# Kernel optimization log

Hardware: AMD Instinct MI355X
Metric: run time of the kernel (lower is better)

The kernel has to match this reference:

```python
import jax, jax.numpy as jnp
import numpy as np

NUM_EXPERTS = 256
TOP_K = 8
N_GROUP = 8
TOPK_GROUP = 4
ROUTED_SCALING = 2.5
EXPERTS_PER_GROUP = NUM_EXPERTS // N_GROUP  # 32


def setup_inputs() -> dict:
    key = jax.random.key(0)
    k1, k2, k3 = jax.random.split(key, 3)
    hidden_states = jax.random.normal(k1, (8192, 7168), dtype=jnp.float32)
    weight = jax.random.normal(k2, (NUM_EXPERTS, 7168), dtype=jnp.float32) * 0.02
    e_score_correction_bias = jax.random.normal(k3, (NUM_EXPERTS,), dtype=jnp.float32) * 0.1
    return {
        "hidden_states": hidden_states,
        "weight": weight,
        "e_score_correction_bias": e_score_correction_bias,
    }


def reference(hidden_states, weight, e_score_correction_bias):
    # Router logits: [T, E]
    router_logits = jnp.einsum("th,eh->te", hidden_states, weight)
    scores = jax.nn.sigmoid(router_logits)
    scores_for_choice = scores + e_score_correction_bias  # [T, E]

    T = scores_for_choice.shape[0]
    # Group-limited selection (noaux_tc): group score = sum of top-2 experts in group
    grouped = scores_for_choice.reshape(T, N_GROUP, EXPERTS_PER_GROUP)
    group_top2, _ = jax.lax.top_k(grouped, 2)            # [T, G, 2]
    group_scores = group_top2.sum(axis=-1)               # [T, G]
    _, group_idx = jax.lax.top_k(group_scores, TOPK_GROUP)  # [T, topk_group]
    group_mask = jax.nn.one_hot(group_idx, N_GROUP, dtype=scores.dtype).max(axis=1)  # [T, G]
    expert_mask = jnp.repeat(group_mask, EXPERTS_PER_GROUP, axis=-1)  # [T, E]
    masked_scores = scores_for_choice * expert_mask

    # Final top-k experts; routing weights gathered from raw sigmoid scores
    _, selected_experts = jax.lax.top_k(masked_scores, TOP_K)         # [T, K] int32
    routing_weights = jnp.take_along_axis(scores, selected_experts, axis=-1)  # [T, K]
    routing_weights = routing_weights / (routing_weights.sum(axis=-1, keepdims=True) + 1e-20)
    routing_weights = routing_weights * ROUTED_SCALING
    return routing_weights, selected_experts
```

## Files before the change

kernel.cpp:

```cpp
#include <hip/hip_runtime.h>
#include <math.h>
#include <stdint.h>

#define T_TOK 8192
#define NEXP  256
#define HD    7168
#define PLANE ((size_t)T_TOK * NEXP)
#define SCALE 4096.0f
#define INV_S2 (1.0f / 16777216.0f)
#define BM 128
#define BK 32
#define NSTEP_TOT (HD / BK)
#define BIMG_STEP 32768

typedef _Float16 h8  __attribute__((ext_vector_type(8)));
typedef float f32x16 __attribute__((ext_vector_type(16)));
typedef __attribute__((address_space(3))) uint8_t       lds_t;
typedef __attribute__((address_space(1))) const uint8_t gbl_t;

__global__ __launch_bounds__(256) void wconv(const float* __restrict__ W,
                                             _Float16* __restrict__ img) {
  const int cc  = blockIdx.x * 256 + threadIdx.x;
  const int t   = cc >> 11;
  const int c   = cc & 2047;
  const int hl  = c >> 10;
  const int rem = c & 1023;
  const int row = rem >> 2;
  const int sp  = rem & 3;
  const int sl  = sp ^ ((row >> 1) & 3);
  const int k   = t * BK + sl * 8;

  const float* src = W + (size_t)row * HD + k;
  const float4 v0 = *(const float4*)src;
  const float4 v1 = *(const float4*)(src + 4);
  const float xs[8] = {v0.x, v0.y, v0.z, v0.w, v1.x, v1.y, v1.z, v1.w};
  h8 out;
#pragma unroll
  for (int j = 0; j < 8; ++j) {
    const float v = xs[j] * SCALE;
    const _Float16 hh = (_Float16)v;
    out[j] = hl ? (_Float16)(v - (float)hh) : hh;
  }
  *(h8*)(img + (size_t)cc * 8) = out;
}

__global__ __launch_bounds__(512, 2) void router_gemm(
    const float* __restrict__ X, const _Float16* __restrict__ img,
    float* __restrict__ partial, int S) {
  __shared__ __align__(1024) _Float16 As[2][2][BM][BK];
  __shared__ __align__(1024) _Float16 Bs[2][2][NEXP][BK];

  const int tid = threadIdx.x;
  const int id  = blockIdx.x;
  const int sb  = id % S;
  const int mb  = id / S;

  const int row0  = mb * BM;
  const int nstep = (HD / S) / BK;
  const int tbase = sb * nstep;

  const int lane = tid & 63, wv = tid >> 6;
  const int wm = wv >> 2, wn = wv & 3;
  const int r31 = lane & 31, kg = lane >> 5;

  const int sm = tid >> 2;
  const int sk = tid & 3;
  const int spA = sk ^ ((sm >> 1) & 3);

  const float* Ap = X + (size_t)(row0 + sm) * HD + tbase * BK + sk * 8;
  const uint8_t* imgB = (const uint8_t*)img + (size_t)tbase * BIMG_STEP + tid * 16;

  f32x16 accP[2][2], accQ[2][2];
#pragma unroll
  for (int i = 0; i < 2; ++i)
#pragma unroll
    for (int j = 0; j < 2; ++j) { accP[i][j] = (f32x16)(0.f); accQ[i][j] = (f32x16)(0.f); }

#define STAGE_B(t, b)                                                          \
  {                                                                            \
    const uint8_t* g = imgB + (size_t)(t) * BIMG_STEP;                         \
    uint8_t* l = (uint8_t*)&Bs[b][0][0][0] + tid * 16;                         \
    _Pragma("unroll")                                                          \
    for (int i = 0; i < 4; ++i)                                                \
      __builtin_amdgcn_global_load_lds((gbl_t*)(uintptr_t)(g + i * 8192),      \
                                       (lds_t*)(uintptr_t)(l + i * 8192),      \
                                       16, 0, 0);                              \
  }

#define CVT_WRITE_A(b, va, vb)                                                 \
  {                                                                            \
    const float xs[8] = {va.x, va.y, va.z, va.w, vb.x, vb.y, vb.z, vb.w};      \
    h8 hv, lv_;                                                                \
    _Pragma("unroll")                                                          \
    for (int j = 0; j < 8; ++j) {                                              \
      const float v = xs[j] * SCALE;                                           \
      const _Float16 hh = (_Float16)v;                                         \
      hv[j] = hh; lv_[j] = (_Float16)(v - (float)hh);                          \
    }                                                                          \
    *(h8*)&As[b][0][sm][spA * 8] = hv;                                         \
    *(h8*)&As[b][1][sm][spA * 8] = lv_;                                        \
  }

  {
    const float4 a0 = *(const float4*)(Ap);
    const float4 a1 = *(const float4*)(Ap + 4);
    __builtin_amdgcn_sched_barrier(0);
    STAGE_B(0, 0);
    asm volatile("s_waitcnt vmcnt(0)" ::: "memory");
    __builtin_amdgcn_sched_barrier(0);
    CVT_WRITE_A(0, a0, a1);
    asm volatile("s_waitcnt lgkmcnt(0)" ::: "memory");
    __builtin_amdgcn_s_barrier();
  }

  for (int t = 0; t < nstep; ++t) {
    const int cur = t & 1;
    const int nxt = cur ^ 1;
    const bool more = (t + 1 < nstep);

    float4 a0, a1;
    if (more) {
      const float* ap = Ap + (size_t)(t + 1) * BK;
      a0 = *(const float4*)(ap);
      a1 = *(const float4*)(ap + 4);
      __builtin_amdgcn_sched_barrier(0);
      STAGE_B(t + 1, nxt);
      __builtin_amdgcn_sched_barrier(0);
      asm volatile("s_waitcnt vmcnt(6)" ::: "memory");
    } else {
      asm volatile("s_waitcnt vmcnt(0)" ::: "memory");
    }
    __builtin_amdgcn_sched_barrier(0);

    h8 aH[2][2], aL[2][2], bH[2][2], bL[2][2];
#pragma unroll
    for (int ks = 0; ks < 2; ++ks) {
#pragma unroll
      for (int mi = 0; mi < 2; ++mi) {
        const int row = wm * 64 + mi * 32 + r31;
        const int sp  = (ks * 2 + kg) ^ ((row >> 1) & 3);
        aH[ks][mi] = *(const h8*)&As[cur][0][row][sp * 8];
        aL[ks][mi] = *(const h8*)&As[cur][1][row][sp * 8];
      }
#pragma unroll
      for (int ni = 0; ni < 2; ++ni) {
        const int col = wn * 64 + ni * 32 + r31;
        const int sp  = (ks * 2 + kg) ^ ((col >> 1) & 3);
        bH[ks][ni] = *(const h8*)&Bs[cur][0][col][sp * 8];
        bL[ks][ni] = *(const h8*)&Bs[cur][1][col][sp * 8];
      }
    }
    asm volatile("s_waitcnt lgkmcnt(0)" ::: "memory");
    __builtin_amdgcn_sched_barrier(0);

    __builtin_amdgcn_s_setprio(1);
#pragma unroll
    for (int ks = 0; ks < 2; ++ks) {
#pragma unroll
      for (int mi = 0; mi < 2; ++mi)
#pragma unroll
        for (int ni = 0; ni < 2; ++ni)
          accP[mi][ni] = __builtin_amdgcn_mfma_f32_32x32x16_f16(aH[ks][mi], bH[ks][ni], accP[mi][ni], 0, 0, 0);
#pragma unroll
      for (int mi = 0; mi < 2; ++mi)
#pragma unroll
        for (int ni = 0; ni < 2; ++ni)
          accQ[mi][ni] = __builtin_amdgcn_mfma_f32_32x32x16_f16(aL[ks][mi], bH[ks][ni], accQ[mi][ni], 0, 0, 0);
#pragma unroll
      for (int mi = 0; mi < 2; ++mi)
#pragma unroll
        for (int ni = 0; ni < 2; ++ni)
          accQ[mi][ni] = __builtin_amdgcn_mfma_f32_32x32x16_f16(aH[ks][mi], bL[ks][ni], accQ[mi][ni], 0, 0, 0);
    }
    __builtin_amdgcn_s_setprio(0);

    if (more) {
      asm volatile("s_waitcnt vmcnt(4)" ::: "memory");
      __builtin_amdgcn_sched_barrier(0);
      CVT_WRITE_A(nxt, a0, a1);
    }
    asm volatile("s_waitcnt lgkmcnt(0)" ::: "memory");
    __builtin_amdgcn_s_barrier();
  }

  float* base = partial + (size_t)sb * PLANE;
#pragma unroll
  for (int mi = 0; mi < 2; ++mi)
#pragma unroll
    for (int ni = 0; ni < 2; ++ni) {
      const f32x16 acc = accP[mi][ni] + accQ[mi][ni];
      const int col = wn * 64 + ni * 32 + r31;
#pragma unroll
      for (int reg = 0; reg < 16; ++reg) {
        const int rr  = (reg & 3) + 8 * (reg >> 2) + 4 * kg;
        const int row = row0 + wm * 64 + mi * 32 + rr;
        base[(size_t)row * NEXP + col] = acc[reg];
      }
    }
}

__global__ __launch_bounds__(256) void gate_kernel(const float* __restrict__ logits,
                                                   const float* __restrict__ bias,
                                                   float* __restrict__ out_w,
                                                   float* __restrict__ out_e, int S) {
    const int wave = threadIdx.x >> 6;
    const int lane = threadIdx.x & 63;
    const int t = blockIdx.x * 4 + wave;
    if (t >= T_TOK) return;

    float l4[4] = {0.f, 0.f, 0.f, 0.f};
    for (int s = 0; s < S; ++s) {
        const float4 v = *(const float4*)(&logits[(size_t)s * PLANE + (size_t)t * NEXP + lane * 4]);
        l4[0] += v.x; l4[1] += v.y; l4[2] += v.z; l4[3] += v.w;
    }
    const float4 bv = *(const float4*)(&bias[lane * 4]);

    float s4[4], c[4];
#pragma unroll
    for (int j = 0; j < 4; ++j) s4[j] = 1.f / (1.f + expf(-l4[j] * INV_S2));
    c[0] = s4[0] + bv.x;
    c[1] = s4[1] + bv.y;
    c[2] = s4[2] + bv.z;
    c[3] = s4[3] + bv.w;

    float a = fmaxf(c[0], c[1]), b = fminf(c[0], c[1]);
    float d = fmaxf(c[2], c[3]), e = fminf(c[2], c[3]);
    float m1 = fmaxf(a, d);
    float m2 = fmaxf(fminf(a, d), fmaxf(b, e));
#pragma unroll
    for (int off = 1; off < 8; off <<= 1) {
        const float o1 = __shfl_xor(m1, off);
        const float o2 = __shfl_xor(m2, off);
        const float n1 = fmaxf(m1, o1);
        const float n2 = fmaxf(fminf(m1, o1), fmaxf(m2, o2));
        m1 = n1; m2 = n2;
    }
    const float gs = m1 + m2;
    const int   g  = lane >> 3;

    int rank = 0;
#pragma unroll
    for (int gg = 0; gg < 8; ++gg) {
        const float og = __shfl(gs, gg * 8);
        rank += (og > gs) || (og == gs && gg < g);
    }
    const bool gsel = rank < 4;

    float v[4];
#pragma unroll
    for (int j = 0; j < 4; ++j) v[j] = gsel ? c[j] : 0.0f;

    float selw = 0.f;
    int   seli = 0;
    float wsum = 0.f;

#pragma unroll
    for (int k = 0; k < 8; ++k) {
        float bvv = v[0]; int bi = lane * 4; float br = s4[0];
#pragma unroll
        for (int j = 1; j < 4; ++j) {
            if (v[j] > bvv) { bvv = v[j]; bi = lane * 4 + j; br = s4[j]; }
        }
#pragma unroll
        for (int off = 32; off > 0; off >>= 1) {
            const float ov = __shfl_xor(bvv, off);
            const int   oi = __shfl_xor(bi, off);
            const float orr = __shfl_xor(br, off);
            if (ov > bvv || (ov == bvv && oi < bi)) { bvv = ov; bi = oi; br = orr; }
        }
        if (lane == k) { selw = br; seli = bi; }
        wsum += br;
        const int rem = bi - lane * 4;
#pragma unroll
        for (int j = 0; j < 4; ++j)
            if (rem == j) v[j] = -INFINITY;
    }

    if (lane < 8) {
        const float w = selw / (wsum + 1e-20f) * 2.5f;
        out_w[(size_t)t * 8 + lane] = w;
        out_e[(size_t)t * 8 + lane] = (float)seli;
    }
}

extern "C" void kernel_launch(void* const* d_in, const int* in_sizes, int n_in,
                              void* d_out, int out_size, void* d_ws, size_t ws_size,
                              hipStream_t stream) {
    const float* X    = (const float*)d_in[0];
    const float* W    = (const float*)d_in[1];
    const float* bias = (const float*)d_in[2];
    float* out = (float*)d_out;

    _Float16* img = (_Float16*)d_ws;
    const size_t woff = (size_t)NSTEP_TOT * BIMG_STEP;
    float* partial = (float*)((char*)d_ws + woff);

    int S = 1;
    if (ws_size >= woff + 4 * PLANE * sizeof(float)) S = 4;
    else if (ws_size >= woff + 2 * PLANE * sizeof(float)) S = 2;

    wconv<<<dim3(NSTEP_TOT * 2048 / 256), 256, 0, stream>>>(W, img);
    router_gemm<<<dim3((T_TOK / BM) * S), 512, 0, stream>>>(X, img, partial, S);
    gate_kernel<<<dim3(T_TOK / 4), 256, 0, stream>>>(partial, bias, out, out + (size_t)T_TOK * 8, S);
}
```

Before: 131.2 us.

## Halve GEMM M-tile to 64 rows with 256-thread blocks and split LDS waits

Shrinks the router GEMM block tile from 128 to 64 token rows and drops to 4 waves per block, so each wave now covers all 64 rows and a 64-expert column slice. B staging takes 8 smaller LDS loads per thread. The MFMA sequence is split per k-substep, with a partial lgkmcnt wait so the first half of the MFMAs can start while the second half's LDS reads are still in flight. The vmcnt waits and barrier placement are reworked. This doubles the grid size and halves A reuse of the B tile per block, so global traffic for the weight image per token rises in exchange for more blocks and occupancy.

```diff
diff --git a/kernel.cpp b/kernel.cpp
--- a/kernel.cpp
+++ b/kernel.cpp
@@ -8,7 +8,7 @@
 #define PLANE ((size_t)T_TOK * NEXP)
 #define SCALE 4096.0f
 #define INV_S2 (1.0f / 16777216.0f)
-#define BM 128
+#define BM 64
 #define BK 32
 #define NSTEP_TOT (HD / BK)
 #define BIMG_STEP 32768
@@ -44,7 +44,7 @@
   *(h8*)(img + (size_t)cc * 8) = out;
 }
 
-__global__ __launch_bounds__(512, 2) void router_gemm(
+__global__ __launch_bounds__(256, 2) void router_gemm(
     const float* __restrict__ X, const _Float16* __restrict__ img,
     float* __restrict__ partial, int S) {
   __shared__ __align__(1024) _Float16 As[2][2][BM][BK];
@@ -60,7 +60,6 @@
   const int tbase = sb * nstep;
 
   const int lane = tid & 63, wv = tid >> 6;
-  const int wm = wv >> 2, wn = wv & 3;
   const int r31 = lane & 31, kg = lane >> 5;
 
   const int sm = tid >> 2;
@@ -81,9 +80,9 @@
     const uint8_t* g = imgB + (size_t)(t) * BIMG_STEP;                         \
     uint8_t* l = (uint8_t*)&Bs[b][0][0][0] + tid * 16;                         \
     _Pragma("unroll")                                                          \
-    for (int i = 0; i < 4; ++i)                                                \
-      __builtin_amdgcn_global_load_lds((gbl_t*)(uintptr_t)(g + i * 8192),      \
-                                       (lds_t*)(uintptr_t)(l + i * 8192),      \
+    for (int i = 0; i < 8; ++i)                                                \
+      __builtin_amdgcn_global_load_lds((gbl_t*)(uintptr_t)(g + i * 4096),      \
+                                       (lds_t*)(uintptr_t)(l + i * 4096),      \
                                        16, 0, 0);                              \
   }
 
@@ -126,61 +125,73 @@
       __builtin_amdgcn_sched_barrier(0);
       STAGE_B(t + 1, nxt);
       __builtin_amdgcn_sched_barrier(0);
-      asm volatile("s_waitcnt vmcnt(6)" ::: "memory");
-    } else {
-      asm volatile("s_waitcnt vmcnt(0)" ::: "memory");
-    }
-    __builtin_amdgcn_sched_barrier(0);
+    }
 
     h8 aH[2][2], aL[2][2], bH[2][2], bL[2][2];
 #pragma unroll
     for (int ks = 0; ks < 2; ++ks) {
 #pragma unroll
       for (int mi = 0; mi < 2; ++mi) {
-        const int row = wm * 64 + mi * 32 + r31;
+        const int row = mi * 32 + r31;
         const int sp  = (ks * 2 + kg) ^ ((row >> 1) & 3);
         aH[ks][mi] = *(const h8*)&As[cur][0][row][sp * 8];
         aL[ks][mi] = *(const h8*)&As[cur][1][row][sp * 8];
       }
 #pragma unroll
       for (int ni = 0; ni < 2; ++ni) {
-        const int col = wn * 64 + ni * 32 + r31;
+        const int col = wv * 64 + ni * 32 + r31;
         const int sp  = (ks * 2 + kg) ^ ((col >> 1) & 3);
         bH[ks][ni] = *(const h8*)&Bs[cur][0][col][sp * 8];
         bL[ks][ni] = *(const h8*)&Bs[cur][1][col][sp * 8];
       }
-    }
+      __builtin_amdgcn_sched_barrier(0);
+    }
+
+    asm volatile("s_waitcnt lgkmcnt(8)" ::: "memory");
+    __builtin_amdgcn_sched_barrier(0);
+    __builtin_amdgcn_s_setprio(1);
+#pragma unroll
+    for (int mi = 0; mi < 2; ++mi)
+#pragma unroll
+      for (int ni = 0; ni < 2; ++ni)
+        accP[mi][ni] = __builtin_amdgcn_mfma_f32_32x32x16_f16(aH[0][mi], bH[0][ni], accP[mi][ni], 0, 0, 0);
+#pragma unroll
+    for (int mi = 0; mi < 2; ++mi)
+#pragma unroll
+      for (int ni = 0; ni < 2; ++ni)
+        accQ[mi][ni] = __builtin_amdgcn_mfma_f32_32x32x16_f16(aL[0][mi], bH[0][ni], accQ[mi][ni], 0, 0, 0);
+#pragma unroll
+    for (int mi = 0; mi < 2; ++mi)
+#pragma unroll
+      for (int ni = 0; ni < 2; ++ni)
+        accQ[mi][ni] = __builtin_amdgcn_mfma_f32_32x32x16_f16(aH[0][mi], bL[0][ni], accQ[mi][ni], 0, 0, 0);
+
     asm volatile("s_waitcnt lgkmcnt(0)" ::: "memory");
     __builtin_amdgcn_sched_barrier(0);
-
-    __builtin_amdgcn_s_setprio(1);
-#pragma unroll
-    for (int ks = 0; ks < 2; ++ks) {
-#pragma unroll
-      for (int mi = 0; mi < 2; ++mi)
-#pragma unroll
-        for (int ni = 0; ni < 2; ++ni)
-          accP[mi][ni] = __builtin_amdgcn_mfma_f32_32x32x16_f16(aH[ks][mi], bH[ks][ni], accP[mi][ni], 0, 0, 0);
-#pragma unroll
-      for (int mi = 0; mi < 2; ++mi)
-#pragma unroll
-        for (int ni = 0; ni < 2; ++ni)
-          accQ[mi][ni] = __builtin_amdgcn_mfma_f32_32x32x16_f16(aL[ks][mi], bH[ks][ni], accQ[mi][ni], 0, 0, 0);
-#pragma unroll
-      for (int mi = 0; mi < 2; ++mi)
-#pragma unroll
-        for (int ni = 0; ni < 2; ++ni)
-          accQ[mi][ni] = __builtin_amdgcn_mfma_f32_32x32x16_f16(aH[ks][mi], bL[ks][ni], accQ[mi][ni], 0, 0, 0);
-    }
+#pragma unroll
+    for (int mi = 0; mi < 2; ++mi)
+#pragma unroll
+      for (int ni = 0; ni < 2; ++ni)
+        accP[mi][ni] = __builtin_amdgcn_mfma_f32_32x32x16_f16(aH[1][mi], bH[1][ni], accP[mi][ni], 0, 0, 0);
+#pragma unroll
+    for (int mi = 0; mi < 2; ++mi)
+#pragma unroll
+      for (int ni = 0; ni < 2; ++ni)
+        accQ[mi][ni] = __builtin_amdgcn_mfma_f32_32x32x16_f16(aL[1][mi], bH[1][ni], accQ[mi][ni], 0, 0, 0);
+#pragma unroll
+    for (int mi = 0; mi < 2; ++mi)
+#pragma unroll
+      for (int ni = 0; ni < 2; ++ni)
+        accQ[mi][ni] = __builtin_amdgcn_mfma_f32_32x32x16_f16(aH[1][mi], bL[1][ni], accQ[mi][ni], 0, 0, 0);
     __builtin_amdgcn_s_setprio(0);
 
     if (more) {
-      asm volatile("s_waitcnt vmcnt(4)" ::: "memory");
+      asm volatile("s_waitcnt vmcnt(8)" ::: "memory");
       __builtin_amdgcn_sched_barrier(0);
       CVT_WRITE_A(nxt, a0, a1);
-    }
-    asm volatile("s_waitcnt lgkmcnt(0)" ::: "memory");
-    __builtin_amdgcn_s_barrier();
+      asm volatile("s_waitcnt vmcnt(0) lgkmcnt(0)" ::: "memory");
+      __builtin_amdgcn_s_barrier();
+    }
   }
 
   float* base = partial + (size_t)sb * PLANE;
@@ -189,11 +200,11 @@
 #pragma unroll
     for (int ni = 0; ni < 2; ++ni) {
       const f32x16 acc = accP[mi][ni] + accQ[mi][ni];
-      const int col = wn * 64 + ni * 32 + r31;
+      const int col = wv * 64 + ni * 32 + r31;
 #pragma unroll
       for (int reg = 0; reg < 16; ++reg) {
         const int rr  = (reg & 3) + 8 * (reg >> 2) + 4 * kg;
-        const int row = row0 + wm * 64 + mi * 32 + rr;
+        const int row = row0 + mi * 32 + rr;
         base[(size_t)row * NEXP + col] = acc[reg];
       }
     }
@@ -300,6 +311,6 @@
     else if (ws_size >= woff + 2 * PLANE * sizeof(float)) S = 2;
 
     wconv<<<dim3(NSTEP_TOT * 2048 / 256), 256, 0, stream>>>(W, img);
-    router_gemm<<<dim3((T_TOK / BM) * S), 512, 0, stream>>>(X, img, partial, S);
+    router_gemm<<<dim3((T_TOK / BM) * S), 256, 0, stream>>>(X, img, partial, S);
     gate_kernel<<<dim3(T_TOK / 4), 256, 0, stream>>>(partial, bias, out, out + (size_t)T_TOK * 8, S);
 }
```

Measured after the change: 143.5 us. +9.4%, slower.
